# Kernel optimization log

Hardware: AMD Instinct MI355X
Metric: run time of the kernel (lower is better)

Reference implementation:

```python
import jax, jax.numpy as jnp
import numpy as np


def setup_inputs() -> dict:
    key = jax.random.key(0)
    ks = jax.random.split(key, 5)
    B, S, F = 32, 2048, 64
    s = lambda d: 1.0 / np.sqrt(d)
    return {
        "x": jax.random.normal(ks[0], (B, S, F), jnp.float32),
        "Wq": jax.random.normal(ks[1], (F, 24), jnp.float32) * s(F),
        "Wk": jax.random.normal(ks[2], (F, 24), jnp.float32) * s(F),
        "Wv": jax.random.normal(ks[3], (F, 32), jnp.float32) * s(F),
        "Wh": jax.random.normal(ks[4], (32, F), jnp.float32) * s(32),
    }


def reference(x, Wq, Wk, Wv, Wh):
    # x: [B, S, F]
    q = jnp.einsum("bsf,fd->bsd", x, Wq)  # [B, S, 24]
    k = jnp.einsum("bsf,fd->bsd", x, Wk)  # [B, S, 24]
    v = jnp.einsum("bsf,fd->bsd", x, Wv)  # [B, S, 32]
    a = jnp.einsum("bqd,bkd->bqk", q, k)  # [B, S, S]
    # NOTE: softmax over dim=1 (query axis), as in the original module
    a = jax.nn.softmax(a, axis=1)
    h1 = jnp.einsum("bqk,bkd->bqd", a, v)  # [B, S, 32]
    return jnp.einsum("bsd,df->bsf", h1, Wh)  # [B, S, F]
```

## Files before the change

kernel.cpp:

```cpp
#include <hip/hip_runtime.h>
#include <hip/hip_fp16.h>

#define SS 2048
#define L2E 1.44269504088896340736f

typedef _Float16 f16x4 __attribute__((ext_vector_type(4)));
typedef _Float16 f16x8 __attribute__((ext_vector_type(8)));
typedef float f32x4 __attribute__((ext_vector_type(4)));

#define GLDS16(g, l) __builtin_amdgcn_global_load_lds(                          \
    (const __attribute__((address_space(1))) void*)(g),                         \
    (__attribute__((address_space(3))) void*)(l), 16, 0, 0)
#define GLDS4(g, l) __builtin_amdgcn_global_load_lds(                           \
    (const __attribute__((address_space(1))) void*)(g),                         \
    (__attribute__((address_space(3))) void*)(l), 4, 0, 0)

__global__ __launch_bounds__(256) void qkv_kernel(
    const float* __restrict__ x, const float* __restrict__ Wq,
    const float* __restrict__ Wk, const float* __restrict__ Wv,
    _Float16* __restrict__ qfp, _Float16* __restrict__ kfp,
    _Float16* __restrict__ vfp)
{
    __shared__ float xs[64 * 65];
    __shared__ float wc[64 * 80];
    __shared__ __align__(16) _Float16 os[3 * 2048];

    int t = threadIdx.x;
    for (int i = t; i < 64 * 80; i += 256) {
        int f = i / 80, c = i % 80;
        float v;
        if (c < 24) v = Wq[f * 24 + c];
        else if (c < 48) v = Wk[f * 24 + (c - 24)];
        else v = Wv[f * 32 + (c - 48)];
        wc[i] = v;
    }
    long rowbase = (long)blockIdx.x * 64;
    const float4* xg = (const float4*)(x + rowbase * 64);
    for (int i = t; i < 64 * 16; i += 256) {
        int r = i >> 4, c4 = i & 15;
        float4 v = xg[i];
        xs[r * 65 + c4 * 4 + 0] = v.x;
        xs[r * 65 + c4 * 4 + 1] = v.y;
        xs[r * 65 + c4 * 4 + 2] = v.z;
        xs[r * 65 + c4 * 4 + 3] = v.w;
    }
    if (t < 128) {
        int reg = t >> 6, rr = t & 63;
        *(f16x8*)&os[reg * 2048 + (rr >> 4) * 512 + (48 + (rr & 15)) * 8]
            = (f16x8){0, 0, 0, 0, 0, 0, 0, 0};
    }
    __syncthreads();

    int rg = t >> 4;
    int cg = t & 15;
    float acc[4][5];
    #pragma unroll
    for (int j = 0; j < 4; ++j)
        #pragma unroll
        for (int i = 0; i < 5; ++i) acc[j][i] = 0.f;

    #pragma unroll 8
    for (int f = 0; f < 64; ++f) {
        float xv[4];
        #pragma unroll
        for (int j = 0; j < 4; ++j) xv[j] = xs[(rg * 4 + j) * 65 + f];
        #pragma unroll
        for (int i = 0; i < 5; ++i) {
            float w = wc[f * 80 + cg * 5 + i];
            #pragma unroll
            for (int j = 0; j < 4; ++j) acc[j][i] += xv[j] * w;
        }
    }

    int st_l = rg >> 2;
    int slb  = (rg & 3) * 4;
    #pragma unroll
    for (int j = 0; j < 4; ++j) {
        int sl = slb + j;
        #pragma unroll
        for (int i = 0; i < 5; ++i) {
            int c = cg * 5 + i;
            if (c < 24) {
                os[st_l * 512 + ((c >> 3) * 16 + sl) * 8 + (c & 7)]
                    = (_Float16)(acc[j][i] * L2E);
            } else if (c < 48) {
                int ck = c - 24;
                os[2048 + st_l * 512 + ((ck >> 3) * 16 + sl) * 8 + (ck & 7)]
                    = (_Float16)acc[j][i];
            } else {
                int vd = c - 48;
                os[4096 + st_l * 512 + (vd >> 4) * 256
                   + ((rg & 3) * 16 + (vd & 15)) * 4 + j] = (_Float16)acc[j][i];
            }
        }
    }
    __syncthreads();

    long blk = blockIdx.x;
    *(f16x8*)(qfp + blk * 2048 + t * 8) = *(const f16x8*)&os[t * 8];
    *(f16x8*)(kfp + blk * 2048 + t * 8) = *(const f16x8*)&os[2048 + t * 8];
    *(f16x8*)(vfp + blk * 2048 + t * 8) = *(const f16x8*)&os[4096 + t * 8];
}

__global__ __launch_bounds__(256) void stats_kernel(
    const _Float16* __restrict__ qf, const _Float16* __restrict__ kf,
    float* __restrict__ zpart)
{
    int w = blockIdx.x;
    int b = w & 31, kb = (w >> 5) & 7, qs = w >> 8;
    int t = threadIdx.x;
    int wv = t >> 6, l = t & 63, llo = l & 15, lhi = l >> 4;

    const _Float16* kfb = kf + ((long)b * 128 + kb * 16 + wv * 4) * 512 + l * 8;
    f16x8 af[4];
    #pragma unroll
    for (int kt = 0; kt < 4; ++kt) af[kt] = *(const f16x8*)(kfb + kt * 512);

    const _Float16* qb = qf + ((long)b * 128 + qs * 16) * 512 + l * 8;
    f32x4 z[4] = {{0,0,0,0},{0,0,0,0},{0,0,0,0},{0,0,0,0}};

    #pragma unroll 4
    for (int qi = 0; qi < 16; ++qi) {
        f16x8 q0 = *(const f16x8*)(qb + qi * 512);
        #pragma unroll
        for (int kt = 0; kt < 4; ++kt) {
            f32x4 d = __builtin_amdgcn_mfma_f32_16x16x32_f16(af[kt], q0,
                        (f32x4){0,0,0,0}, 0, 0, 0);
            #pragma unroll
            for (int r = 0; r < 4; ++r) z[kt][r] += __builtin_amdgcn_exp2f(d[r]);
        }
    }
    #pragma unroll
    for (int m = 1; m < 16; m <<= 1)
        #pragma unroll
        for (int kt = 0; kt < 4; ++kt)
            #pragma unroll
            for (int r = 0; r < 4; ++r) z[kt][r] += __shfl_xor(z[kt][r], m, 64);
    if (llo == 0) {
        #pragma unroll
        for (int kt = 0; kt < 4; ++kt)
            *(f32x4*)(zpart + ((long)qs * 32 + b) * SS + kb * 256 + wv * 64
                      + kt * 16 + lhi * 4) = z[kt];
    }
}

__global__ __launch_bounds__(256) void finalize_kernel(
    const float* __restrict__ zpart, float* __restrict__ wneg)
{
    int i = blockIdx.x * 256 + threadIdx.x;
    float s = 0.f;
    #pragma unroll
    for (int qs = 0; qs < 8; ++qs) s += zpart[(long)qs * 32 * SS + i];
    wneg[i] = -__builtin_amdgcn_logf(s);
}

__global__ __launch_bounds__(256) void attn_out_kernel(
    const _Float16* __restrict__ qf, const _Float16* __restrict__ kf,
    const _Float16* __restrict__ vf, const float* __restrict__ wneg,
    const float* __restrict__ Wh, float* __restrict__ out)
{
    __shared__ __align__(16) _Float16 lds[2][4224];

    int w = blockIdx.x;
    int b = w & 31, qblk = w >> 5;
    int t = threadIdx.x;
    int wv = t >> 6, l = t & 63, llo = l & 15, lhi = l >> 4;
    int q0 = qblk * 64 + wv * 16;

    f16x8 qfr = *(const f16x8*)(qf + ((long)b * 128 + qblk * 4 + wv) * 512 + l * 8);

    f16x4 whlo[4], whhi[4];
    #pragma unroll
    for (int fb = 0; fb < 4; ++fb)
        #pragma unroll
        for (int j = 0; j < 4; ++j) {
            whlo[fb][j] = (_Float16)Wh[(4 * lhi + j) * 64 + fb * 16 + llo];
            whhi[fb][j] = (_Float16)Wh[(16 + 4 * lhi + j) * 64 + fb * 16 + llo];
        }

    const _Float16* kgb = kf + ((long)b * 128 + wv) * 512 + l * 8;
    const _Float16* vgb = vf + ((long)b * 32) * 2048 + wv * 512 + l * 8;
    const float*    wgb = wneg + (long)b * SS + l;

    f32x4 acc0 = {0,0,0,0}, acc1 = {0,0,0,0};

    GLDS16(kgb, &lds[0][wv * 512]);
    GLDS16(vgb, &lds[0][2048 + wv * 512]);
    if (wv == 0) GLDS4(wgb, (float*)&lds[0][4096]);

    for (int tile = 0; tile < 32; ++tile) {
        int cb = tile & 1;
        __syncthreads();
        if (tile < 31) {
            GLDS16(kgb + (long)(tile + 1) * 2048, &lds[cb ^ 1][wv * 512]);
            GLDS16(vgb + (long)(tile + 1) * 2048, &lds[cb ^ 1][2048 + wv * 512]);
            if (wv == 0) GLDS4(wgb + (tile + 1) * 64, (float*)&lds[cb ^ 1][4096]);
        }
        const _Float16* Kb = &lds[cb][0];
        const _Float16* Vb = &lds[cb][2048];
        const float*    Wb = (const float*)&lds[cb][4096];
        #pragma unroll
        for (int t4 = 0; t4 < 4; ++t4) {
            f16x8 kfr = *(const f16x8*)(Kb + t4 * 512 + l * 8);
            float4 w4 = *(const float4*)(Wb + t4 * 16 + lhi * 4);
            f32x4 d = __builtin_amdgcn_mfma_f32_16x16x32_f16(kfr, qfr,
                        (f32x4){w4.x, w4.y, w4.z, w4.w}, 0, 0, 0);
            f16x4 pa;
            #pragma unroll
            for (int r = 0; r < 4; ++r) pa[r] = (_Float16)__builtin_amdgcn_exp2f(d[r]);
            f16x4 v0 = *(const f16x4*)(Vb + t4 * 512 + l * 4);
            f16x4 v1 = *(const f16x4*)(Vb + t4 * 512 + 256 + l * 4);
            acc0 = __builtin_amdgcn_mfma_f32_16x16x16f16(v0, pa, acc0, 0, 0, 0);
            acc1 = __builtin_amdgcn_mfma_f32_16x16x16f16(v1, pa, acc1, 0, 0, 0);
        }
    }

    f16x4 h0, h1;
    #pragma unroll
    for (int r = 0; r < 4; ++r) {
        h0[r] = (_Float16)acc0[r];
        h1[r] = (_Float16)acc1[r];
    }
    float* orow = out + ((long)b * SS + q0 + llo) * 64 + 4 * lhi;
    #pragma unroll
    for (int fb = 0; fb < 4; ++fb) {
        f32x4 o = __builtin_amdgcn_mfma_f32_16x16x16f16(whlo[fb], h0,
                    (f32x4){0,0,0,0}, 0, 0, 0);
        o = __builtin_amdgcn_mfma_f32_16x16x16f16(whhi[fb], h1, o, 0, 0, 0);
        *(f32x4*)(orow + fb * 16) = o;
    }
}

extern "C" void kernel_launch(void* const* d_in, const int* in_sizes, int n_in,
                              void* d_out, int out_size, void* d_ws, size_t ws_size,
                              hipStream_t stream) {
    const float* x  = (const float*)d_in[0];
    const float* Wq = (const float*)d_in[1];
    const float* Wk = (const float*)d_in[2];
    const float* Wv = (const float*)d_in[3];
    const float* Wh = (const float*)d_in[4];
    float* out = (float*)d_out;

    char* ws = (char*)d_ws;
    _Float16* qf  = (_Float16*)(ws);
    _Float16* kf  = (_Float16*)(ws + (4l << 20));
    _Float16* vf  = (_Float16*)(ws + (8l << 20));
    float* wneg   = (float*)(ws + (12l << 20));
    float* zpart  = (float*)(ws + (12l << 20) + (256l << 10));

    qkv_kernel<<<1024, 256, 0, stream>>>(x, Wq, Wk, Wv, qf, kf, vf);
    stats_kernel<<<2048, 256, 0, stream>>>(qf, kf, zpart);
    finalize_kernel<<<256, 256, 0, stream>>>(zpart, wneg);
    attn_out_kernel<<<1024, 256, 0, stream>>>(qf, kf, vf, wneg, Wh, out);
}
```

Baseline: 83.82 us.

## Restructure QKV, stats and attention kernels for more register reuse

The QKV projection now uses transposed x in LDS with vectorized weight loads, 2x12 register tiles, and the output staging buffer aliased onto the weight buffer. The V layout changes so each lane reads both halves as one 8-wide load. The stats kernel gives each wave 8 key tiles and streams q through a double-buffered LDS copy, halving the grid. The attention kernel splits keys across waves, with each wave covering all four query groups straight from global memory, then reduces partial results through LDS before the Wh projection. These changes target load and synchronization overhead, at the cost of more registers, a cross-wave reduction and changed block-to-batch mapping.

New measurement: 150.2 us. 1.79x slower.

```diff
diff --git a/kernel.cpp b/kernel.cpp
--- a/kernel.cpp
+++ b/kernel.cpp
@@ -11,9 +11,6 @@
 #define GLDS16(g, l) __builtin_amdgcn_global_load_lds(                          \
     (const __attribute__((address_space(1))) void*)(g),                         \
     (__attribute__((address_space(3))) void*)(l), 16, 0, 0)
-#define GLDS4(g, l) __builtin_amdgcn_global_load_lds(                           \
-    (const __attribute__((address_space(1))) void*)(g),                         \
-    (__attribute__((address_space(3))) void*)(l), 4, 0, 0)
 
 __global__ __launch_bounds__(256) void qkv_kernel(
     const float* __restrict__ x, const float* __restrict__ Wq,
@@ -21,76 +18,89 @@
     _Float16* __restrict__ qfp, _Float16* __restrict__ kfp,
     _Float16* __restrict__ vfp)
 {
-    __shared__ float xs[64 * 65];
-    __shared__ float wc[64 * 80];
-    __shared__ __align__(16) _Float16 os[3 * 2048];
+    __shared__ float xsT[64 * 64];
+    __shared__ float wc[64 * 96];
 
     int t = threadIdx.x;
-    for (int i = t; i < 64 * 80; i += 256) {
-        int f = i / 80, c = i % 80;
-        float v;
-        if (c < 24) v = Wq[f * 24 + c];
-        else if (c < 48) v = Wk[f * 24 + (c - 24)];
-        else v = Wv[f * 32 + (c - 48)];
-        wc[i] = v;
+    for (int i = t; i < 384; i += 256) {
+        float4 v = ((const float4*)Wq)[i];
+        int f = (i * 4) / 24, c = (i * 4) % 24;
+        *(float4*)&wc[f * 96 + c] = v;
+    }
+    for (int i = t; i < 384; i += 256) {
+        float4 v = ((const float4*)Wk)[i];
+        int f = (i * 4) / 24, c = (i * 4) % 24;
+        *(float4*)&wc[f * 96 + 24 + c] = v;
+    }
+    for (int i = t; i < 512; i += 256) {
+        float4 v = ((const float4*)Wv)[i];
+        int f = i >> 3, c = (i * 4) & 31;
+        *(float4*)&wc[f * 96 + 48 + c] = v;
+    }
+    {
+        int f = t >> 2, seg = t & 3;
+        *(float4*)&wc[f * 96 + 80 + seg * 4] = (float4){0.f, 0.f, 0.f, 0.f};
     }
     long rowbase = (long)blockIdx.x * 64;
     const float4* xg = (const float4*)(x + rowbase * 64);
-    for (int i = t; i < 64 * 16; i += 256) {
+    for (int i = t; i < 1024; i += 256) {
         int r = i >> 4, c4 = i & 15;
         float4 v = xg[i];
-        xs[r * 65 + c4 * 4 + 0] = v.x;
-        xs[r * 65 + c4 * 4 + 1] = v.y;
-        xs[r * 65 + c4 * 4 + 2] = v.z;
-        xs[r * 65 + c4 * 4 + 3] = v.w;
-    }
+        xsT[(c4 * 4 + 0) * 64 + r] = v.x;
+        xsT[(c4 * 4 + 1) * 64 + r] = v.y;
+        xsT[(c4 * 4 + 2) * 64 + r] = v.z;
+        xsT[(c4 * 4 + 3) * 64 + r] = v.w;
+    }
+    __syncthreads();
+
+    int rg = t >> 3;
+    int cg = t & 7;
+    float acc0[12], acc1[12];
+    #pragma unroll
+    for (int i = 0; i < 12; ++i) acc0[i] = acc1[i] = 0.f;
+
+    #pragma unroll 4
+    for (int f = 0; f < 64; ++f) {
+        float2 xv = *(const float2*)&xsT[f * 64 + rg * 2];
+        const float* wr = &wc[f * 96 + cg * 12];
+        float4 wA = *(const float4*)(wr);
+        float4 wB = *(const float4*)(wr + 4);
+        float4 wC = *(const float4*)(wr + 8);
+        float wv_[12] = {wA.x, wA.y, wA.z, wA.w, wB.x, wB.y, wB.z, wB.w,
+                         wC.x, wC.y, wC.z, wC.w};
+        #pragma unroll
+        for (int i = 0; i < 12; ++i) {
+            acc0[i] += xv.x * wv_[i];
+            acc1[i] += xv.y * wv_[i];
+        }
+    }
+    __syncthreads();
+    _Float16* os = (_Float16*)wc;
+
     if (t < 128) {
         int reg = t >> 6, rr = t & 63;
         *(f16x8*)&os[reg * 2048 + (rr >> 4) * 512 + (48 + (rr & 15)) * 8]
             = (f16x8){0, 0, 0, 0, 0, 0, 0, 0};
     }
-    __syncthreads();
-
-    int rg = t >> 4;
-    int cg = t & 15;
-    float acc[4][5];
-    #pragma unroll
-    for (int j = 0; j < 4; ++j)
-        #pragma unroll
-        for (int i = 0; i < 5; ++i) acc[j][i] = 0.f;
-
-    #pragma unroll 8
-    for (int f = 0; f < 64; ++f) {
-        float xv[4];
-        #pragma unroll
-        for (int j = 0; j < 4; ++j) xv[j] = xs[(rg * 4 + j) * 65 + f];
-        #pragma unroll
-        for (int i = 0; i < 5; ++i) {
-            float w = wc[f * 80 + cg * 5 + i];
-            #pragma unroll
-            for (int j = 0; j < 4; ++j) acc[j][i] += xv[j] * w;
-        }
-    }
-
-    int st_l = rg >> 2;
-    int slb  = (rg & 3) * 4;
-    #pragma unroll
-    for (int j = 0; j < 4; ++j) {
-        int sl = slb + j;
-        #pragma unroll
-        for (int i = 0; i < 5; ++i) {
-            int c = cg * 5 + i;
+
+    #pragma unroll
+    for (int j = 0; j < 2; ++j) {
+        int s = rg * 2 + j, st = s >> 4;
+        const float* a = j ? acc1 : acc0;
+        #pragma unroll
+        for (int i = 0; i < 12; ++i) {
+            int c = cg * 12 + i;
             if (c < 24) {
-                os[st_l * 512 + ((c >> 3) * 16 + sl) * 8 + (c & 7)]
-                    = (_Float16)(acc[j][i] * L2E);
+                os[st * 512 + ((c >> 3) * 16 + (s & 15)) * 8 + (c & 7)]
+                    = (_Float16)(a[i] * L2E);
             } else if (c < 48) {
                 int ck = c - 24;
-                os[2048 + st_l * 512 + ((ck >> 3) * 16 + sl) * 8 + (ck & 7)]
-                    = (_Float16)acc[j][i];
-            } else {
+                os[2048 + st * 512 + ((ck >> 3) * 16 + (s & 15)) * 8 + (ck & 7)]
+                    = (_Float16)a[i];
+            } else if (c < 80) {
                 int vd = c - 48;
-                os[4096 + st_l * 512 + (vd >> 4) * 256
-                   + ((rg & 3) * 16 + (vd & 15)) * 4 + j] = (_Float16)acc[j][i];
+                os[4096 + st * 512 + (((s >> 2) & 3) * 16 + (vd & 15)) * 8
+                   + (vd >> 4) * 4 + (s & 3)] = (_Float16)a[i];
             }
         }
     }
@@ -106,41 +116,47 @@
     const _Float16* __restrict__ qf, const _Float16* __restrict__ kf,
     float* __restrict__ zpart)
 {
+    __shared__ __align__(16) _Float16 qbuf[2][1024];
     int w = blockIdx.x;
-    int b = w & 31, kb = (w >> 5) & 7, qs = w >> 8;
+    int b = w >> 5, kb = (w >> 3) & 3, qs = w & 7;
     int t = threadIdx.x;
     int wv = t >> 6, l = t & 63, llo = l & 15, lhi = l >> 4;
 
-    const _Float16* kfb = kf + ((long)b * 128 + kb * 16 + wv * 4) * 512 + l * 8;
-    f16x8 af[4];
-    #pragma unroll
-    for (int kt = 0; kt < 4; ++kt) af[kt] = *(const f16x8*)(kfb + kt * 512);
-
-    const _Float16* qb = qf + ((long)b * 128 + qs * 16) * 512 + l * 8;
-    f32x4 z[4] = {{0,0,0,0},{0,0,0,0},{0,0,0,0},{0,0,0,0}};
-
-    #pragma unroll 4
-    for (int qi = 0; qi < 16; ++qi) {
-        f16x8 q0 = *(const f16x8*)(qb + qi * 512);
-        #pragma unroll
-        for (int kt = 0; kt < 4; ++kt) {
-            f32x4 d = __builtin_amdgcn_mfma_f32_16x16x32_f16(af[kt], q0,
-                        (f32x4){0,0,0,0}, 0, 0, 0);
+    const _Float16* kfb = kf + ((long)b * 128 + kb * 32 + wv * 8) * 512 + l * 8;
+    f16x8 af[8];
+    #pragma unroll
+    for (int j = 0; j < 8; ++j) af[j] = *(const f16x8*)(kfb + j * 512);
+
+    const _Float16* qsrc = qf + ((long)b * 128 + qs * 16) * 512 + l * 8;
+    f32x4 z[8];
+    #pragma unroll
+    for (int j = 0; j < 8; ++j) z[j] = (f32x4){0.f, 0.f, 0.f, 0.f};
+
+    if (wv == 0) GLDS16(qsrc, &qbuf[0][0]);
+    for (int it = 0; it < 16; ++it) {
+        int cb = it & 1;
+        __syncthreads();
+        if (wv == 0 && it < 15) GLDS16(qsrc + (it + 1) * 512, &qbuf[cb ^ 1][0]);
+        f16x8 q0 = *(const f16x8*)&qbuf[cb][l * 8];
+        #pragma unroll
+        for (int j = 0; j < 8; ++j) {
+            f32x4 d = __builtin_amdgcn_mfma_f32_16x16x32_f16(af[j], q0,
+                        (f32x4){0.f, 0.f, 0.f, 0.f}, 0, 0, 0);
             #pragma unroll
-            for (int r = 0; r < 4; ++r) z[kt][r] += __builtin_amdgcn_exp2f(d[r]);
+            for (int r = 0; r < 4; ++r) z[j][r] += __builtin_amdgcn_exp2f(d[r]);
         }
     }
     #pragma unroll
     for (int m = 1; m < 16; m <<= 1)
         #pragma unroll
-        for (int kt = 0; kt < 4; ++kt)
+        for (int j = 0; j < 8; ++j)
             #pragma unroll
-            for (int r = 0; r < 4; ++r) z[kt][r] += __shfl_xor(z[kt][r], m, 64);
+            for (int r = 0; r < 4; ++r) z[j][r] += __shfl_xor(z[j][r], m, 64);
     if (llo == 0) {
         #pragma unroll
-        for (int kt = 0; kt < 4; ++kt)
-            *(f32x4*)(zpart + ((long)qs * 32 + b) * SS + kb * 256 + wv * 64
-                      + kt * 16 + lhi * 4) = z[kt];
+        for (int j = 0; j < 8; ++j)
+            *(f32x4*)(zpart + ((long)qs * 32 + b) * SS + kb * 512 + wv * 128
+                      + j * 16 + lhi * 4) = z[j];
     }
 }
 
@@ -154,80 +170,82 @@
     wneg[i] = -__builtin_amdgcn_logf(s);
 }
 
-__global__ __launch_bounds__(256) void attn_out_kernel(
+__global__ __launch_bounds__(256, 4) void attn_out_kernel(
     const _Float16* __restrict__ qf, const _Float16* __restrict__ kf,
     const _Float16* __restrict__ vf, const float* __restrict__ wneg,
     const float* __restrict__ Wh, float* __restrict__ out)
 {
-    __shared__ __align__(16) _Float16 lds[2][4224];
-
+    __shared__ f32x4 red[4][8][64];
     int w = blockIdx.x;
-    int b = w & 31, qblk = w >> 5;
+    int b = w >> 5, qblk = w & 31;
     int t = threadIdx.x;
     int wv = t >> 6, l = t & 63, llo = l & 15, lhi = l >> 4;
-    int q0 = qblk * 64 + wv * 16;
-
-    f16x8 qfr = *(const f16x8*)(qf + ((long)b * 128 + qblk * 4 + wv) * 512 + l * 8);
-
-    f16x4 whlo[4], whhi[4];
-    #pragma unroll
-    for (int fb = 0; fb < 4; ++fb)
-        #pragma unroll
-        for (int j = 0; j < 4; ++j) {
-            whlo[fb][j] = (_Float16)Wh[(4 * lhi + j) * 64 + fb * 16 + llo];
-            whhi[fb][j] = (_Float16)Wh[(16 + 4 * lhi + j) * 64 + fb * 16 + llo];
-        }
-
-    const _Float16* kgb = kf + ((long)b * 128 + wv) * 512 + l * 8;
-    const _Float16* vgb = vf + ((long)b * 32) * 2048 + wv * 512 + l * 8;
-    const float*    wgb = wneg + (long)b * SS + l;
-
-    f32x4 acc0 = {0,0,0,0}, acc1 = {0,0,0,0};
-
-    GLDS16(kgb, &lds[0][wv * 512]);
-    GLDS16(vgb, &lds[0][2048 + wv * 512]);
-    if (wv == 0) GLDS4(wgb, (float*)&lds[0][4096]);
-
-    for (int tile = 0; tile < 32; ++tile) {
-        int cb = tile & 1;
-        __syncthreads();
-        if (tile < 31) {
-            GLDS16(kgb + (long)(tile + 1) * 2048, &lds[cb ^ 1][wv * 512]);
-            GLDS16(vgb + (long)(tile + 1) * 2048, &lds[cb ^ 1][2048 + wv * 512]);
-            if (wv == 0) GLDS4(wgb + (tile + 1) * 64, (float*)&lds[cb ^ 1][4096]);
-        }
-        const _Float16* Kb = &lds[cb][0];
-        const _Float16* Vb = &lds[cb][2048];
-        const float*    Wb = (const float*)&lds[cb][4096];
-        #pragma unroll
-        for (int t4 = 0; t4 < 4; ++t4) {
-            f16x8 kfr = *(const f16x8*)(Kb + t4 * 512 + l * 8);
-            float4 w4 = *(const float4*)(Wb + t4 * 16 + lhi * 4);
-            f32x4 d = __builtin_amdgcn_mfma_f32_16x16x32_f16(kfr, qfr,
-                        (f32x4){w4.x, w4.y, w4.z, w4.w}, 0, 0, 0);
+
+    const _Float16* qb = qf + ((long)b * 128 + qblk * 4) * 512 + l * 8;
+    f16x8 qv[4];
+    #pragma unroll
+    for (int g = 0; g < 4; ++g) qv[g] = *(const f16x8*)(qb + g * 512);
+
+    const _Float16* kg = kf + ((long)b * 128 + wv * 32) * 512 + l * 8;
+    const _Float16* vg = vf + ((long)b * 128 + wv * 32) * 512 + l * 8;
+    const float*    wg = wneg + (long)b * SS + wv * 512 + lhi * 4;
+
+    f32x4 acc[4][2];
+    #pragma unroll
+    for (int g = 0; g < 4; ++g) {
+        acc[g][0] = (f32x4){0.f, 0.f, 0.f, 0.f};
+        acc[g][1] = (f32x4){0.f, 0.f, 0.f, 0.f};
+    }
+
+    #pragma unroll 2
+    for (int i = 0; i < 32; ++i) {
+        f16x8 kfr = *(const f16x8*)(kg + i * 512);
+        float4 w4 = *(const float4*)(wg + i * 16);
+        f16x8 v01 = *(const f16x8*)(vg + i * 512);
+        f32x4 cw = {w4.x, w4.y, w4.z, w4.w};
+        f16x4 v0 = {v01[0], v01[1], v01[2], v01[3]};
+        f16x4 v1 = {v01[4], v01[5], v01[6], v01[7]};
+        #pragma unroll
+        for (int g = 0; g < 4; ++g) {
+            f32x4 d = __builtin_amdgcn_mfma_f32_16x16x32_f16(kfr, qv[g], cw, 0, 0, 0);
             f16x4 pa;
             #pragma unroll
             for (int r = 0; r < 4; ++r) pa[r] = (_Float16)__builtin_amdgcn_exp2f(d[r]);
-            f16x4 v0 = *(const f16x4*)(Vb + t4 * 512 + l * 4);
-            f16x4 v1 = *(const f16x4*)(Vb + t4 * 512 + 256 + l * 4);
-            acc0 = __builtin_amdgcn_mfma_f32_16x16x16f16(v0, pa, acc0, 0, 0, 0);
-            acc1 = __builtin_amdgcn_mfma_f32_16x16x16f16(v1, pa, acc1, 0, 0, 0);
-        }
-    }
-
-    f16x4 h0, h1;
-    #pragma unroll
-    for (int r = 0; r < 4; ++r) {
-        h0[r] = (_Float16)acc0[r];
-        h1[r] = (_Float16)acc1[r];
-    }
-    float* orow = out + ((long)b * SS + q0 + llo) * 64 + 4 * lhi;
-    #pragma unroll
-    for (int fb = 0; fb < 4; ++fb) {
-        f32x4 o = __builtin_amdgcn_mfma_f32_16x16x16f16(whlo[fb], h0,
-                    (f32x4){0,0,0,0}, 0, 0, 0);
-        o = __builtin_amdgcn_mfma_f32_16x16x16f16(whhi[fb], h1, o, 0, 0, 0);
-        *(f32x4*)(orow + fb * 16) = o;
+            acc[g][0] = __builtin_amdgcn_mfma_f32_16x16x16f16(v0, pa, acc[g][0], 0, 0, 0);
+            acc[g][1] = __builtin_amdgcn_mfma_f32_16x16x16f16(v1, pa, acc[g][1], 0, 0, 0);
+        }
+    }
+
+    #pragma unroll
+    for (int g = 0; g < 4; ++g) {
+        red[wv][g * 2][l]     = acc[g][0];
+        red[wv][g * 2 + 1][l] = acc[g][1];
+    }
+    __syncthreads();
+
+    f16x4 wlo, whi;
+    #pragma unroll
+    for (int j = 0; j < 4; ++j) {
+        wlo[j] = (_Float16)Wh[(4 * lhi + j) * 64 + wv * 16 + llo];
+        whi[j] = (_Float16)Wh[(16 + 4 * lhi + j) * 64 + wv * 16 + llo];
+    }
+    long q0 = (long)b * SS + qblk * 64;
+    #pragma unroll
+    for (int g = 0; g < 4; ++g) {
+        f32x4 s0 = red[0][g * 2][l] + red[1][g * 2][l]
+                 + red[2][g * 2][l] + red[3][g * 2][l];
+        f32x4 s1 = red[0][g * 2 + 1][l] + red[1][g * 2 + 1][l]
+                 + red[2][g * 2 + 1][l] + red[3][g * 2 + 1][l];
+        f16x4 h0, h1;
+        #pragma unroll
+        for (int r = 0; r < 4; ++r) {
+            h0[r] = (_Float16)s0[r];
+            h1[r] = (_Float16)s1[r];
+        }
+        f32x4 o = __builtin_amdgcn_mfma_f32_16x16x16f16(wlo, h0,
+                    (f32x4){0.f, 0.f, 0.f, 0.f}, 0, 0, 0);
+        o = __builtin_amdgcn_mfma_f32_16x16x16f16(whi, h1, o, 0, 0, 0);
+        *(f32x4*)(out + (q0 + g * 16 + llo) * 64 + wv * 16 + 4 * lhi) = o;
     }
 }
 
@@ -249,7 +267,7 @@
     float* zpart  = (float*)(ws + (12l << 20) + (256l << 10));
 
     qkv_kernel<<<1024, 256, 0, stream>>>(x, Wq, Wk, Wv, qf, kf, vf);
-    stats_kernel<<<2048, 256, 0, stream>>>(qf, kf, zpart);
+    stats_kernel<<<1024, 256, 0, stream>>>(qf, kf, zpart);
     finalize_kernel<<<256, 256, 0, stream>>>(zpart, wneg);
     attn_out_kernel<<<1024, 256, 0, stream>>>(qf, kf, vf, wneg, Wh, out);
 }
```
